# Optimization experiments

Measured on AMD Instinct MI355X. Metric: run time of the kernel, lower is better.

The kernel has to match this reference:

```python
import jax, jax.numpy as jnp
import numpy as np

K, M_EMB, N_HID, D_CTX, D_ATT, M_COV = 128, 256, 256, 684, 512, 256
B, H, W = 64, 16, 48


def gru_cell(x, h, W_ih, W_hh, b_ih, b_hh):
    # PyTorch GRUCell semantics
    gi = x @ W_ih.T + b_ih
    gh = h @ W_hh.T + b_hh
    i_r, i_z, i_n = jnp.split(gi, 3, axis=-1)
    h_r, h_z, h_n = jnp.split(gh, 3, axis=-1)
    r = jax.nn.sigmoid(i_r + h_r)
    z = jax.nn.sigmoid(i_z + h_z)
    n = jnp.tanh(i_n + r * h_n)
    return (1.0 - z) * n + z * h


def setup_inputs() -> dict:
    key = jax.random.key(0)
    ks = jax.random.split(key, 24)
    s = 0.02
    inp = {
        'y': jax.random.randint(ks[0], (B,), 0, K),
        'y_mask': jnp.ones((B,), jnp.float32),
        'context': jax.random.normal(ks[1], (B, D_CTX, H, W), jnp.float32),
        'pre_hidden': jax.random.normal(ks[2], (B, N_HID), jnp.float32),
        'alpha_past': jax.random.uniform(ks[3], (B, H, W), jnp.float32),
        'emb': jax.random.normal(ks[4], (K + 1, M_EMB)) * s,
        'W_ih1': jax.random.normal(ks[5], (3 * N_HID, M_EMB)) * s,
        'W_hh1': jax.random.normal(ks[6], (3 * N_HID, N_HID)) * s,
        'b_ih1': jnp.zeros((3 * N_HID,)),
        'b_hh1': jnp.zeros((3 * N_HID,)),
        'conv_Ua_w': jax.random.normal(ks[7], (D_ATT, D_CTX, 1, 1)) * s,
        'conv_Ua_b': jnp.zeros((D_ATT,)),
        'Wa': jax.random.normal(ks[8], (D_ATT, N_HID)) * s,
        'conv_Q_w': jax.random.normal(ks[9], (M_COV, 1, 3, 3)) * s,
        'Uf': jax.random.normal(ks[10], (D_ATT, M_COV)) * s,
        'Uf_b': jnp.zeros((D_ATT,)),
        'va': jax.random.normal(ks[11], (1, D_ATT)) * s,
        'va_b': jnp.zeros((1,)),
        'W_ih2': jax.random.normal(ks[12], (3 * N_HID, D_CTX)) * s,
        'W_hh2': jax.random.normal(ks[13], (3 * N_HID, N_HID)) * s,
        'b_ih2': jnp.zeros((3 * N_HID,)),
        'b_hh2': jnp.zeros((3 * N_HID,)),
        'Wct': jax.random.normal(ks[14], (M_EMB, D_CTX)) * s,
        'Wct_b': jnp.zeros((M_EMB,)),
        'Wht': jax.random.normal(ks[15], (M_EMB, N_HID)) * s,
        'Wht_b': jnp.zeros((M_EMB,)),
        'W0': jax.random.normal(ks[16], (K, M_EMB // 2)) * s,
        'W0_b': jnp.zeros((K,)),
    }
    return inp


def reference(y, y_mask, context, pre_hidden, alpha_past, emb,
              W_ih1, W_hh1, b_ih1, b_hh1, conv_Ua_w, conv_Ua_b, Wa,
              conv_Q_w, Uf, Uf_b, va, va_b,
              W_ih2, W_hh2, b_ih2, b_hh2, Wct, Wct_b, Wht, Wht_b, W0, W0_b):
    embedded = emb[y]                                           # [B, m]
    s_hat = gru_cell(embedded, pre_hidden, W_ih1, W_hh1, b_ih1, b_hh1)
    s_hat = y_mask[:, None] * s_hat + (1.0 - y_mask)[:, None] * pre_hidden

    Wa_h1 = s_hat @ Wa.T                                        # [B, A]
    # 1x1 conv == channel projection, output in NHWC layout
    Ua_ctx = jnp.einsum('bdhw,ad->bhwa', context, conv_Ua_w[:, :, 0, 0]) + conv_Ua_b
    # 3x3 coverage conv over past attention map
    cover_F = jax.lax.conv_general_dilated(
        alpha_past[:, None, :, :], conv_Q_w, (1, 1), 'SAME',
        dimension_numbers=('NCHW', 'OIHW', 'NCHW'))              # [B, M, H, W]
    cover_F = jnp.transpose(cover_F, (0, 2, 3, 1))               # [B, H, W, M]
    cover_vector = cover_F @ Uf.T + Uf_b                         # [B, H, W, A]

    e_att = jnp.tanh(Ua_ctx + Wa_h1[:, None, None, :] + cover_vector)
    alpha = (e_att @ va.T + va_b)[..., 0].reshape(e_att.shape[0], -1)  # [B, H*W]
    alpha = jax.nn.softmax(alpha, axis=1)

    ct = jnp.einsum('bdp,bp->bd', context.reshape(context.shape[0], context.shape[1], -1), alpha)

    s = gru_cell(ct, s_hat, W_ih2, W_hh2, b_ih2, b_hh2)
    s = y_mask[:, None] * s + (1.0 - y_mask)[:, None] * s_hat

    logit = ct @ Wct.T + Wct_b + s @ Wht.T + Wht_b + embedded    # [B, m]
    logit = logit.reshape(logit.shape[0], -1, 2).max(axis=2)     # maxout -> [B, m/2]
    out = logit @ W0.T + W0_b                                    # [B, K]
    return out, s, alpha.reshape(alpha.shape[0], H, W)
```

## Files before the change

### kernel.cpp

```cpp
#include <hip/hip_runtime.h>
#include <hip/hip_bf16.h>
#include <math.h>

#define BB 64
#define KV 128
#define ME 256
#define NH 256
#define DC 684
#define DA 512
#define MC 256
#define HH_ 16
#define WW_ 48
#define HW_ 768
#define NS 22

typedef __attribute__((ext_vector_type(8))) short bf16x8;
typedef __attribute__((ext_vector_type(4))) float f32x4;

#define WS_G     0
#define WS_RB    (WS_G + 4608)
#define WS_EMB   (WS_RB + 32768)
#define WS_SH    (WS_EMB + 16384)
#define WS_AL    (WS_SH + 16384)
#define WS_CT    (WS_AL + 49152)
#define WS_APACK (WS_CT + 43776)
#define WS_GI    (WS_APACK + 180224)
#define WS_GH    (WS_GI + 49152)
#define WS_LG    WS_GI
#define WS_BP    (WS_GH + 49152)
#define NEED_BYTES ((size_t)441600 * 4 + (size_t)34603008 * 2)

static __device__ __forceinline__ unsigned short f2b(float v) {
    __hip_bfloat16 h = __float2bfloat16(v);
    return *reinterpret_cast<unsigned short*>(&h);
}

static __device__ __forceinline__ void gl_lds16(const unsigned short* g,
                                                unsigned short* l) {
    __builtin_amdgcn_global_load_lds(
        (const __attribute__((address_space(1))) unsigned int*)g,
        (__attribute__((address_space(3))) unsigned int*)l, 16, 0, 0);
}

__global__ __launch_bounds__(512) void k_prep(
    const float* __restrict__ ctx, const float* __restrict__ Ua,
    const float* __restrict__ Uf, const float* __restrict__ convQ,
    const int* __restrict__ y, const float* __restrict__ emb,
    unsigned short* __restrict__ Bpack, unsigned short* __restrict__ Apack,
    float* __restrict__ G, float* __restrict__ embedded) {
    __shared__ unsigned short Ts[64 * 360];
    int bx = blockIdx.x, t = threadIdx.x;
    if (bx < 768) {
        int b = bx / 12, pt = bx % 12, p0 = pt * 64;
        int w = t >> 6, p = t & 63;
        unsigned short* dst = Bpack + (long)(b * 12 + pt) * 22 * 2048;
        for (int ch = 0; ch < 2; ch++) {
            int dbase = ch * 352;
            if (ch) __syncthreads();
#pragma unroll
            for (int iter = 0; iter < 11; iter++) {
                int d0 = dbase + iter * 32 + w * 4;
                float v0 = 0.f, v1 = 0.f, v2 = 0.f, v3 = 0.f;
                const float* src = ctx + ((long)b * DC + d0) * HW_ + p0 + p;
                if (d0 + 0 < DC) v0 = __builtin_nontemporal_load(src);
                if (d0 + 1 < DC) v1 = __builtin_nontemporal_load(src + HW_);
                if (d0 + 2 < DC) v2 = __builtin_nontemporal_load(src + 2 * HW_);
                if (d0 + 3 < DC) v3 = __builtin_nontemporal_load(src + 3 * HW_);
                unsigned u01 = (unsigned)f2b(v0) | ((unsigned)f2b(v1) << 16);
                unsigned u23 = (unsigned)f2b(v2) | ((unsigned)f2b(v3) << 16);
                *(uint2*)&Ts[p * 360 + (d0 - dbase)] = make_uint2(u01, u23);
            }
            __syncthreads();
            int so = t >> 8;
            int tt = t & 255;
            int pp = tt >> 2, slot = tt & 3;
#pragma unroll
            for (int s2 = 0; s2 < 12; s2 += 2) {
                int sl = s2 + so;
                if (sl < 11) {
                    int s = ch * 11 + sl;
                    bf16x8 v = *(const bf16x8*)&Ts[pp * 360 + sl * 32 +
                                                   ((slot ^ ((pp >> 1) & 3))
                                                    << 3)];
                    *(bf16x8*)(dst + (long)(s * 256 + tt) * 8) = v;
                }
            }
        }
    } else if (bx < 856) {
        int bi = bx - 768;
#pragma unroll
        for (int r = 0; r < 8; r++) {
            int idx = bi * 4096 + r * 512 + t;
            int e = idx & 7, slot = (idx >> 3) & 3;
            int a = (idx >> 5) & 511, s = idx >> 14;
            int d = s * 32 + ((slot ^ ((a >> 1) & 3)) << 3) + e;
            float v = (d < DC) ? Ua[a * DC + d] : 0.f;
            Apack[idx] = f2b(v);
        }
    } else if (bx < 865) {
        int idx = (bx - 856) * 512 + t;
        if (idx < DA * 9) {
            int a = idx / 9, k = idx % 9;
            float s = 0.f;
            for (int m = 0; m < MC; m++) s += Uf[a * MC + m] * convQ[m * 9 + k];
            G[idx] = s;
        }
    } else {
        int b = bx - 865;
        if (t < ME) embedded[b * ME + t] = emb[y[b] * ME + t];
    }
}

__global__ __launch_bounds__(256) void k_G(const float* __restrict__ Uf,
                                           const float* __restrict__ convQ,
                                           float* __restrict__ G) {
    int idx = blockIdx.x * 256 + threadIdx.x;
    if (idx >= DA * 9) return;
    int a = idx / 9, k = idx % 9;
    float s = 0.f;
    for (int m = 0; m < MC; m++) s += Uf[a * MC + m] * convQ[m * 9 + k];
    G[idx] = s;
}

__global__ __launch_bounds__(256) void k_prepA(const float* __restrict__ Ua,
                                               unsigned short* __restrict__ Apack) {
    int idx = blockIdx.x * 256 + threadIdx.x;
    if (idx >= NS * DA * 32) return;
    int e = idx & 7, slot = (idx >> 3) & 3;
    int a = (idx >> 5) & 511, s = idx >> 14;
    int d = s * 32 + ((slot ^ ((a >> 1) & 3)) << 3) + e;
    float v = (d < DC) ? Ua[a * DC + d] : 0.f;
    Apack[idx] = f2b(v);
}

__global__ __launch_bounds__(256) void k_emb(const int* __restrict__ y,
                                             const float* __restrict__ emb,
                                             float* __restrict__ embedded) {
    int b = blockIdx.x, t = threadIdx.x;
    embedded[b * ME + t] = emb[y[b] * ME + t];
}

__global__ __launch_bounds__(256) void k_rows256(
    const float* __restrict__ X, const float* __restrict__ W,
    const float* __restrict__ bias, const float* __restrict__ bias2,
    float* __restrict__ out, int outStride) {
    __shared__ float Xs[64 * 257];
    __shared__ float Ws[4 * 260];
    int t = threadIdx.x, w = t >> 6, lane = t & 63;
    for (int i = t; i < 64 * 256; i += 256) {
        int bb = i >> 8, k = i & 255;
        Xs[bb * 257 + k] = X[bb * 256 + k];
    }
    int r = blockIdx.x * 4 + w;
    *(f32x4*)(Ws + w * 260 + lane * 4) = *(const f32x4*)(W + r * 256 + lane * 4);
    __syncthreads();
    const float* xrow = Xs + lane * 257;
    const float* wrow = Ws + w * 260;
    float acc = 0.f;
#pragma unroll 8
    for (int k = 0; k < 256; k++) acc += wrow[k] * xrow[k];
    acc += bias[r];
    if (bias2) acc += bias2[r];
    out[lane * outStride + r] = acc;
}

__global__ __launch_bounds__(256) void k_gih1(
    const float* __restrict__ embedded, const float* __restrict__ pre_hidden,
    const float* __restrict__ W_ih1, const float* __restrict__ W_hh1,
    const float* __restrict__ b_ih1, const float* __restrict__ b_hh1,
    float* __restrict__ gi, float* __restrict__ gh) {
    __shared__ float Xs[64 * 257];
    __shared__ float Ws[4 * 260];
    int bx = blockIdx.x, t = threadIdx.x, w = t >> 6, lane = t & 63;
    const float *X, *W, *bias;
    float* outp;
    int r;
    if (bx < 192) {
        X = embedded; W = W_ih1; bias = b_ih1; outp = gi; r = bx * 4 + w;
    } else {
        X = pre_hidden; W = W_hh1; bias = b_hh1; outp = gh; r = (bx - 192) * 4 + w;
    }
    for (int i = t; i < 64 * 256; i += 256) {
        int bb = i >> 8, k = i & 255;
        Xs[bb * 257 + k] = X[bb * 256 + k];
    }
    *(f32x4*)(Ws + w * 260 + lane * 4) = *(const f32x4*)(W + r * 256 + lane * 4);
    __syncthreads();
    const float* xrow = Xs + lane * 257;
    const float* wrow = Ws + w * 260;
    float acc = 0.f;
#pragma unroll 8
    for (int k = 0; k < 256; k++) acc += wrow[k] * xrow[k];
    outp[lane * 768 + r] = acc + bias[r];
}

__global__ __launch_bounds__(256) void k_gih2(
    const float* __restrict__ ctv, const float* __restrict__ s_hat,
    const float* __restrict__ W_ih2, const float* __restrict__ W_hh2,
    const float* __restrict__ b_ih2, const float* __restrict__ b_hh2,
    float* __restrict__ gi, float* __restrict__ gh) {
    __shared__ float Xs[64 * 257];
    __shared__ float Ws[4 * 260];
    int bx = blockIdx.x, t = threadIdx.x, w = t >> 6, lane = t & 63;
    if (bx < 192) {
        int r = bx * 4 + w;
        float acc = 0.f;
        for (int c = 0; c < 3; c++) {
            int c0 = c * 228;
            __syncthreads();
            for (int i = t; i < 64 * 228; i += 256) {
                int bb = i / 228, kk = i - bb * 228;
                Xs[bb * 229 + kk] = ctv[bb * DC + c0 + kk];
            }
            for (int j = lane; j < 228; j += 64)
                Ws[w * 260 + j] = W_ih2[r * DC + c0 + j];
            __syncthreads();
            const float* xrow = Xs + lane * 229;
            const float* wrow = Ws + w * 260;
#pragma unroll 4
            for (int k = 0; k < 228; k++) acc += wrow[k] * xrow[k];
        }
        gi[lane * 768 + r] = acc + b_ih2[r];
    } else {
        int r = (bx - 192) * 4 + w;
        for (int i = t; i < 64 * 256; i += 256) {
            int bb = i >> 8, k = i & 255;
            Xs[bb * 257 + k] = s_hat[bb * 256 + k];
        }
        *(f32x4*)(Ws + w * 260 + lane * 4) =
            *(const f32x4*)(W_hh2 + r * 256 + lane * 4);
        __syncthreads();
        const float* xrow = Xs + lane * 257;
        const float* wrow = Ws + w * 260;
        float acc = 0.f;
#pragma unroll 8
        for (int k = 0; k < 256; k++) acc += wrow[k] * xrow[k];
        gh[lane * 768 + r] = acc + b_hh2[r];
    }
}

__global__ __launch_bounds__(256) void k_gru(const float* __restrict__ gi,
                                             const float* __restrict__ gh,
                                             const float* __restrict__ h,
                                             const float* __restrict__ y_mask,
                                             float* __restrict__ outp) {
    int b = blockIdx.x, t = threadIdx.x;
    float hv = h[b * NH + t];
    float r = 1.f / (1.f + expf(-(gi[b * 768 + t] + gh[b * 768 + t])));
    float z = 1.f / (1.f + expf(-(gi[b * 768 + 256 + t] + gh[b * 768 + 256 + t])));
    float n = tanhf(gi[b * 768 + 512 + t] + r * gh[b * 768 + 512 + t]);
    float sv = (1.f - z) * n + z * hv;
    float m = y_mask[b];
    outp[b * NH + t] = m * sv + (1.f - m) * hv;
}

__global__ __launch_bounds__(512) void k_att_gl(
    const unsigned short* __restrict__ Apack,
    const unsigned short* __restrict__ Bpack, const float* __restrict__ G,
    const float* __restrict__ rb, const float* __restrict__ va,
    const float* __restrict__ va_b, const float* __restrict__ apast,
    float* __restrict__ alogit) {
    __shared__ __attribute__((aligned(16))) unsigned short lsA[2][16384];
    __shared__ __attribute__((aligned(16))) unsigned short lsB[2][2048];
    __shared__ float ap_s[18 * 50];
    __shared__ float part_s[8][64];
    int pt = blockIdx.x, b = blockIdx.y;
    int t = threadIdx.x, w = t >> 6, lane = t & 63;
    int l15 = lane & 15, lg = lane >> 4;
    int sx = lg ^ ((l15 >> 1) & 3);

    for (int idx = t; idx < 900; idx += 512) {
        int hh = idx / 50, ww = idx % 50;
        float v = 0.f;
        if (hh >= 1 && hh <= HH_ && ww >= 1 && ww <= WW_)
            v = apast[b * HW_ + (hh - 1) * WW_ + (ww - 1)];
        ap_s[idx] = v;
    }

    const unsigned short* Asrc = Apack + w * 2048 + lane * 8;
    const unsigned short* Bsrc =
        Bpack + (long)(b * 12 + pt) * 22 * 2048 + w * 512 + lane * 8;

#define STAGE(S, BUF)                                                        \
    do {                                                                     \
        _Pragma("unroll") for (int i_ = 0; i_ < 4; i_++)                     \
            gl_lds16(Asrc + (long)(S)*16384 + i_ * 512,                      \
                     &lsA[BUF][w * 2048 + i_ * 512]);                        \
        if (w < 4) gl_lds16(Bsrc + (long)(S)*2048, &lsB[BUF][w * 512]);      \
    } while (0)

    f32x4 acc[4][4];
#pragma unroll
    for (int i = 0; i < 4; i++)
#pragma unroll
        for (int j = 0; j < 4; j++) acc[i][j] = {0.f, 0.f, 0.f, 0.f};

    STAGE(0, 0);
    __syncthreads();

    for (int s = 0; s < NS; s++) {
        int cur = s & 1;
        if (s + 1 < NS) STAGE(s + 1, cur ^ 1);
        bf16x8 af[4], bf[4];
#pragma unroll
        for (int j = 0; j < 4; j++)
            bf[j] = *(const bf16x8*)&lsB[cur][(j * 16 + l15) * 32 + sx * 8];
#pragma unroll
        for (int i = 0; i < 4; i++)
            af[i] = *(const bf16x8*)&lsA[cur][(w * 64 + i * 16 + l15) * 32 +
                                              sx * 8];
#pragma unroll
        for (int i = 0; i < 4; i++)
#pragma unroll
            for (int j = 0; j < 4; j++)
                acc[i][j] = __builtin_amdgcn_mfma_f32_16x16x32_bf16(
                    af[i], bf[j], acc[i][j], 0, 0, 0);
        __syncthreads();
    }
#undef STAGE

    float partial[4] = {0.f, 0.f, 0.f, 0.f};
#pragma unroll
    for (int i = 0; i < 4; i++) {
#pragma unroll
        for (int r = 0; r < 4; r++) {
            int a = w * 64 + i * 16 + lg * 4 + r;
            float rbv = rb[b * DA + a];
            float vav = va[a];
            const float* Ga = G + a * 9;
            float g0 = Ga[0], g1 = Ga[1], g2 = Ga[2], g3 = Ga[3], g4 = Ga[4];
            float g5 = Ga[5], g6 = Ga[6], g7 = Ga[7], g8 = Ga[8];
#pragma unroll
            for (int j = 0; j < 4; j++) {
                int p = pt * 64 + j * 16 + l15;
                int hh = p / WW_, ww = p % WW_;
                const float* ap = ap_s + hh * 50 + ww;
                float cov = g0 * ap[0] + g1 * ap[1] + g2 * ap[2] +
                            g3 * ap[50] + g4 * ap[51] + g5 * ap[52] +
                            g6 * ap[100] + g7 * ap[101] + g8 * ap[102];
                float e = tanhf(acc[i][j][r] + rbv + cov);
                partial[j] += vav * e;
            }
        }
    }
#pragma unroll
    for (int j = 0; j < 4; j++) {
        partial[j] += __shfl_xor(partial[j], 16);
        partial[j] += __shfl_xor(partial[j], 32);
    }
    if (lane < 16) {
#pragma unroll
        for (int j = 0; j < 4; j++) part_s[w][j * 16 + lane] = partial[j];
    }
    __syncthreads();
    if (t < 64) {
        float sum = va_b[0];
#pragma unroll
        for (int q = 0; q < 8; q++) sum += part_s[q][t];
        alogit[b * HW_ + pt * 64 + t] = sum;
    }
}

#define LDW 40
__global__ __launch_bounds__(256) void k_att_lds(
    const unsigned short* __restrict__ Apack, const float* __restrict__ ctx,
    const float* __restrict__ G, const float* __restrict__ rb,
    const float* __restrict__ va, const float* __restrict__ va_b,
    const float* __restrict__ apast, float* __restrict__ alogit) {
    __shared__ __attribute__((aligned(16))) short lsB[2][64 * LDW];
    __shared__ float ap_s[18 * 50];
    __shared__ float part_s[4 * 64];
    int b = blockIdx.y;
    int p0 = blockIdx.x * 64;
    int t = threadIdx.x;
    int w = t >> 6, lane = t & 63;
    int l15 = lane & 15, lg = lane >> 4;
    int sxA = lg ^ ((l15 >> 1) & 3);
    int pq = t & 15, kp = t >> 4;
    const float* ctx_b = ctx + (long)b * DC * HW_ + p0;

    for (int idx = t; idx < 900; idx += 256) {
        int hh = idx / 50, ww = idx % 50;
        float v = 0.f;
        if (hh >= 1 && hh <= HH_ && ww >= 1 && ww <= WW_)
            v = apast[b * HW_ + (hh - 1) * WW_ + (ww - 1)];
        ap_s[idx] = v;
    }

#define CTXLOAD(FA, FB, S)                                                   \
    do {                                                                     \
        int d_ = (S) * 32 + 2 * kp;                                          \
        const float* s0_ = ctx_b + (long)d_ * HW_ + pq;                      \
        bool g0_ = d_ < DC, g1_ = (d_ + 1) < DC;                             \
        _Pragma("unroll") for (int j_ = 0; j_ < 4; j_++) {                   \
            FA[j_] = g0_ ? s0_[16 * j_] : 0.f;                               \
            FB[j_] = g1_ ? s0_[HW_ + 16 * j_] : 0.f;                         \
        }                                                                    \
    } while (0)
#define STAGEW(FA, FB, BUF)                                                  \
    do {                                                                     \
        _Pragma("unroll") for (int j_ = 0; j_ < 4; j_++) {                   \
            ((unsigned*)lsB[BUF])[(pq + 16 * j_) * (LDW / 2) + kp] =         \
                (unsigned)f2b(FA[j_]) | ((unsigned)f2b(FB[j_]) << 16);       \
        }                                                                    \
    } while (0)
#define ALOAD(AF, S)                                                         \
    do {                                                                     \
        _Pragma("unroll") for (int i_ = 0; i_ < 8; i_++)                     \
            AF[i_] = *(const bf16x8*)(Apack +                                \
                ((long)((S)*512 + w * 128 + i_ * 16 + l15) * 4 + sxA) * 8);  \
    } while (0)
#define BREAD(BF, BUF)                                                       \
    do {                                                                     \
        _Pragma("unroll") for (int j_ = 0; j_ < 4; j_++)                     \
            BF[j_] = *(const bf16x8*)(&lsB[BUF][(j_ * 16 + l15) * LDW +      \
                                               lg * 8]);                     \
    } while (0)
#define MFMA8x4(AF, BF)                                                      \
    do {                                                                     \
        _Pragma("unroll") for (int i_ = 0; i_ < 8; i_++)                     \
            _Pragma("unroll") for (int j_ = 0; j_ < 4; j_++)                 \
                acc[i_][j_] = __builtin_amdgcn_mfma_f32_16x16x32_bf16(       \
                    AF[i_], BF[j_], acc[i_][j_], 0, 0, 0);                   \
    } while (0)

    f32x4 acc[8][4];
#pragma unroll
    for (int i = 0; i < 8; i++)
#pragma unroll
        for (int j = 0; j < 4; j++) acc[i][j] = {0.f, 0.f, 0.f, 0.f};

    float fa0[4], fb0[4], fa1[4], fb1[4];
    bf16x8 afr0[8], afr1[8], bfr[4];

    CTXLOAD(fa1, fb1, 0);
    ALOAD(afr0, 0);
    STAGEW(fa1, fb1, 0);
    CTXLOAD(fa1, fb1, 1);
    __syncthreads();

    for (int ss = 0; ss < NS; ss += 2) {
        if (ss + 2 < NS) CTXLOAD(fa0, fb0, ss + 2);
        ALOAD(afr1, ss + 1);
        BREAD(bfr, 0);
        STAGEW(fa1, fb1, 1);
        MFMA8x4(afr0, bfr);
        __syncthreads();
        if (ss + 3 < NS) CTXLOAD(fa1, fb1, ss + 3);
        if (ss + 2 < NS) {
            ALOAD(afr0, ss + 2);
            BREAD(bfr, 1);
            STAGEW(fa0, fb0, 0);
            MFMA8x4(afr1, bfr);
        } else {
            BREAD(bfr, 1);
            MFMA8x4(afr1, bfr);
        }
        __syncthreads();
    }

    float partial[4] = {0.f, 0.f, 0.f, 0.f};
#pragma unroll
    for (int i = 0; i < 8; i++) {
#pragma unroll
        for (int r = 0; r < 4; r++) {
            int a = w * 128 + i * 16 + lg * 4 + r;
            float rbv = rb[b * DA + a];
            float vav = va[a];
            const float* Ga = G + a * 9;
            float g0 = Ga[0], g1 = Ga[1], g2 = Ga[2], g3 = Ga[3], g4 = Ga[4];
            float g5 = Ga[5], g6 = Ga[6], g7 = Ga[7], g8 = Ga[8];
#pragma unroll
            for (int j = 0; j < 4; j++) {
                int p = p0 + j * 16 + l15;
                int hh = p / WW_, ww = p % WW_;
                const float* ap = ap_s + hh * 50 + ww;
                float cov = g0 * ap[0] + g1 * ap[1] + g2 * ap[2] +
                            g3 * ap[50] + g4 * ap[51] + g5 * ap[52] +
                            g6 * ap[100] + g7 * ap[101] + g8 * ap[102];
                float e = tanhf(acc[i][j][r] + rbv + cov);
                partial[j] += vav * e;
            }
        }
    }
#pragma unroll
    for (int j = 0; j < 4; j++) {
        partial[j] += __shfl_xor(partial[j], 16);
        partial[j] += __shfl_xor(partial[j], 32);
    }
    if (lane < 16) {
#pragma unroll
        for (int j = 0; j < 4; j++) part_s[w * 64 + j * 16 + lane] = partial[j];
    }
    __syncthreads();
    if (t < 64) {
        float s = va_b[0] + part_s[t] + part_s[64 + t] + part_s[128 + t] +
                  part_s[192 + t];
        alogit[b * HW_ + p0 + t] = s;
    }
}

__global__ __launch_bounds__(256) void k_softmax(const float* __restrict__ alogit,
                                                 float* __restrict__ alpha) {
    __shared__ float red[16];
    int b = blockIdx.x, t = threadIdx.x;
    float v[3];
    float mx = -1e30f;
    for (int i = 0; i < 3; i++) {
        v[i] = alogit[b * HW_ + i * 256 + t];
        mx = fmaxf(mx, v[i]);
    }
    for (int off = 32; off > 0; off >>= 1) mx = fmaxf(mx, __shfl_down(mx, off));
    if ((t & 63) == 0) red[t >> 6] = mx;
    __syncthreads();
    if (t == 0) red[0] = fmaxf(fmaxf(red[0], red[1]), fmaxf(red[2], red[3]));
    __syncthreads();
    mx = red[0];
    float sum = 0.f;
    for (int i = 0; i < 3; i++) {
        v[i] = expf(v[i] - mx);
        sum += v[i];
    }
    for (int off = 32; off > 0; off >>= 1) sum += __shfl_down(sum, off);
    if ((t & 63) == 0) red[8 + (t >> 6)] = sum;
    __syncthreads();
    if (t == 0) red[8] = red[8] + red[9] + red[10] + red[11];
    __syncthreads();
    float inv = 1.f / red[8];
    for (int i = 0; i < 3; i++) alpha[b * HW_ + i * 256 + t] = v[i] * inv;
}

__global__ __launch_bounds__(256) void k_ct_f32(const float* __restrict__ ctx,
                                                const float* __restrict__ alpha,
                                                float* __restrict__ ct) {
    __shared__ float al_s[HW_];
    int b = blockIdx.y;
    int dc0 = blockIdx.x * 114;
    int t = threadIdx.x;
    for (int i = t; i < HW_; i += 256) al_s[i] = alpha[b * HW_ + i];
    __syncthreads();
    int wave = t >> 6, lane = t & 63;
    for (int d = dc0 + wave; d < dc0 + 114; d += 4) {
        const float* row = &ctx[((long)b * DC + d) * HW_];
        float s = 0.f;
#pragma unroll
        for (int q = 0; q < 12; q++) s += row[lane + q * 64] * al_s[lane + q * 64];
        for (int off = 32; off > 0; off >>= 1) s += __shfl_down(s, off);
        if (lane == 0) ct[b * DC + d] = s;
    }
}

__global__ __launch_bounds__(256) void k_logit(
    const float* __restrict__ ctv, const float* __restrict__ s,
    const float* __restrict__ embedded, const float* __restrict__ Wct,
    const float* __restrict__ Wht, const float* __restrict__ Wct_b,
    const float* __restrict__ Wht_b, float* __restrict__ lg) {
    __shared__ float Xs[64 * 257];
    __shared__ float Ws[4 * 232];
    int t = threadIdx.x, w = t >> 6, lane = t & 63;
    int r = blockIdx.x * 4 + w;
    float acc = 0.f;
    for (int c = 0; c < 3; c++) {
        int c0 = c * 228;
        __syncthreads();
        for (int i = t; i < 64 * 228; i += 256) {
            int bb = i / 228, kk = i - bb * 228;
            Xs[bb * 229 + kk] = ctv[bb * DC + c0 + kk];
        }
        for (int j = lane; j < 228; j += 64) Ws[w * 232 + j] = Wct[r * DC + c0 + j];
        __syncthreads();
        const float* xrow = Xs + lane * 229;
        const float* wrow = Ws + w * 232;
#pragma unroll 4
        for (int k = 0; k < 228; k++) acc += wrow[k] * xrow[k];
    }
    __syncthreads();
    for (int i = t; i < 64 * 256; i += 256) {
        int bb = i >> 8, k = i & 255;
        Xs[bb * 257 + k] = s[bb * 256 + k];
    }
    __syncthreads();
    const float* xrow2 = Xs + lane * 257;
    const float* wr = Wht + r * 256;
    float acc2 = 0.f;
#pragma unroll 8
    for (int k = 0; k < 256; k++) acc2 += wr[k] * xrow2[k];
    lg[lane * 256 + r] = acc + acc2 + Wct_b[r] + Wht_b[r] + embedded[lane * 256 + r];
}

__global__ __launch_bounds__(256) void k_head(const float* __restrict__ lg,
                                              const float* __restrict__ W0,
                                              const float* __restrict__ W0_b,
                                              float* __restrict__ out) {
    __shared__ float Xs[64 * 129];
    __shared__ float Ws[4 * 132];
    int t = threadIdx.x, w = t >> 6, lane = t & 63;
    for (int i = t; i < 64 * 128; i += 256) {
        int bb = i >> 7, m = i & 127;
        Xs[bb * 129 + m] = fmaxf(lg[bb * 256 + 2 * m], lg[bb * 256 + 2 * m + 1]);
    }
    int r = blockIdx.x * 4 + w;
    Ws[w * 132 + lane] = W0[r * 128 + lane];
    Ws[w * 132 + 64 + lane] = W0[r * 128 + 64 + lane];
    __syncthreads();
    const float* xrow = Xs + lane * 129;
    const float* wrow = Ws + w * 132;
    float acc = 0.f;
#pragma unroll 8
    for (int k = 0; k < 128; k++) acc += wrow[k] * xrow[k];
    out[lane * KV + r] = acc + W0_b[r];
}

extern "C" void kernel_launch(void* const* d_in, const int* in_sizes, int n_in,
                              void* d_out, int out_size, void* d_ws,
                              size_t ws_size, hipStream_t stream) {
    const int* y = (const int*)d_in[0];
    const float* y_mask = (const float*)d_in[1];
    const float* context = (const float*)d_in[2];
    const float* pre_hidden = (const float*)d_in[3];
    const float* alpha_past = (const float*)d_in[4];
    const float* emb = (const float*)d_in[5];
    const float* W_ih1 = (const float*)d_in[6];
    const float* W_hh1 = (const float*)d_in[7];
    const float* b_ih1 = (const float*)d_in[8];
    const float* b_hh1 = (const float*)d_in[9];
    const float* conv_Ua_w = (const float*)d_in[10];
    const float* conv_Ua_b = (const float*)d_in[11];
    const float* Wa = (const float*)d_in[12];
    const float* conv_Q_w = (const float*)d_in[13];
    const float* Uf = (const float*)d_in[14];
    const float* Uf_b = (const float*)d_in[15];
    const float* va = (const float*)d_in[16];
    const float* va_b = (const float*)d_in[17];
    const float* W_ih2 = (const float*)d_in[18];
    const float* W_hh2 = (const float*)d_in[19];
    const float* b_ih2 = (const float*)d_in[20];
    const float* b_hh2 = (const float*)d_in[21];
    const float* Wct = (const float*)d_in[22];
    const float* Wct_b = (const float*)d_in[23];
    const float* Wht = (const float*)d_in[24];
    const float* Wht_b = (const float*)d_in[25];
    const float* W0 = (const float*)d_in[26];
    const float* W0_b = (const float*)d_in[27];

    float* ws = (float*)d_ws;
    float* out = (float*)d_out;
    float* G = ws + WS_G;
    float* rbias = ws + WS_RB;
    float* embedded = ws + WS_EMB;
    float* s_hat = ws + WS_SH;
    float* alogit = ws + WS_AL;
    float* ctv = ws + WS_CT;
    unsigned short* Apack = (unsigned short*)(ws + WS_APACK);
    float* gi = ws + WS_GI;
    float* gh = ws + WS_GH;
    float* lg = ws + WS_LG;
    unsigned short* Bpack = (unsigned short*)(ws + WS_BP);
    float* s_out = out + 8192;
    float* alpha_out = out + 24576;

    bool fast = ws_size >= NEED_BYTES;

    if (fast) {
        k_prep<<<dim3(929), dim3(512), 0, stream>>>(context, conv_Ua_w, Uf,
                                                    conv_Q_w, y, emb, Bpack,
                                                    Apack, G, embedded);
    } else {
        k_G<<<dim3(18), dim3(256), 0, stream>>>(Uf, conv_Q_w, G);
        k_prepA<<<dim3((NS * DA * 32 + 255) / 256), dim3(256), 0, stream>>>(
            conv_Ua_w, Apack);
        k_emb<<<dim3(64), dim3(256), 0, stream>>>(y, emb, embedded);
    }
    k_gih1<<<dim3(384), dim3(256), 0, stream>>>(embedded, pre_hidden, W_ih1,
                                                W_hh1, b_ih1, b_hh1, gi, gh);
    k_gru<<<dim3(64), dim3(256), 0, stream>>>(gi, gh, pre_hidden, y_mask, s_hat);
    k_rows256<<<dim3(128), dim3(256), 0, stream>>>(s_hat, Wa, conv_Ua_b, Uf_b,
                                                   rbias, 512);
    if (fast) {
        k_att_gl<<<dim3(12, 64), dim3(512), 0, stream>>>(
            Apack, Bpack, G, rbias, va, va_b, alpha_past, alogit);
    } else {
        k_att_lds<<<dim3(12, 64), dim3(256), 0, stream>>>(
            Apack, context, G, rbias, va, va_b, alpha_past, alogit);
    }
    k_softmax<<<dim3(64), dim3(256), 0, stream>>>(alogit, alpha_out);
    k_ct_f32<<<dim3(6, 64), dim3(256), 0, stream>>>(context, alpha_out, ctv);
    k_gih2<<<dim3(384), dim3(256), 0, stream>>>(ctv, s_hat, W_ih2, W_hh2, b_ih2,
                                                b_hh2, gi, gh);
    k_gru<<<dim3(64), dim3(256), 0, stream>>>(gi, gh, s_hat, y_mask, s_out);
    k_logit<<<dim3(64), dim3(256), 0, stream>>>(ctv, s_out, embedded, Wct, Wht,
                                                Wct_b, Wht_b, lg);
    k_head<<<dim3(32), dim3(256), 0, stream>>>(lg, W0, W0_b, out);
}
```

Before: 257.7 us.

## Deepen attention GEMM prefetch with vmcnt waits and fuse softmax into context reduction

The attention GEMM kernel now keeps two stages in flight. It waits with explicit s_waitcnt vmcnt counts and raw barriers instead of a full __syncthreads per step, and all 8 waves issue B loads so every wave has the same counter. Softmax is fused into the ct reduction kernel: each of the 6 blocks per batch recomputes the softmax and only block 0 writes alpha, which removes one launch and an alpha round trip. The context reads in prep drop the nontemporal hint. The main risk is that the hand-set vmcnt values are fragile if the compiler reorders loads, and the softmax work is now repeated six times.

```diff
diff --git a/kernel.cpp b/kernel.cpp
--- a/kernel.cpp
+++ b/kernel.cpp
@@ -62,10 +62,10 @@
                 int d0 = dbase + iter * 32 + w * 4;
                 float v0 = 0.f, v1 = 0.f, v2 = 0.f, v3 = 0.f;
                 const float* src = ctx + ((long)b * DC + d0) * HW_ + p0 + p;
-                if (d0 + 0 < DC) v0 = __builtin_nontemporal_load(src);
-                if (d0 + 1 < DC) v1 = __builtin_nontemporal_load(src + HW_);
-                if (d0 + 2 < DC) v2 = __builtin_nontemporal_load(src + 2 * HW_);
-                if (d0 + 3 < DC) v3 = __builtin_nontemporal_load(src + 3 * HW_);
+                if (d0 + 0 < DC) v0 = src[0];
+                if (d0 + 1 < DC) v1 = src[HW_];
+                if (d0 + 2 < DC) v2 = src[2 * HW_];
+                if (d0 + 3 < DC) v3 = src[3 * HW_];
                 unsigned u01 = (unsigned)f2b(v0) | ((unsigned)f2b(v1) << 16);
                 unsigned u23 = (unsigned)f2b(v2) | ((unsigned)f2b(v3) << 16);
                 *(uint2*)&Ts[p * 360 + (d0 - dbase)] = make_uint2(u01, u23);
@@ -254,7 +254,7 @@
     outp[b * NH + t] = m * sv + (1.f - m) * hv;
 }
 
-__global__ __launch_bounds__(512) void k_att_gl(
+__global__ __launch_bounds__(512) void k_att_cnt(
     const unsigned short* __restrict__ Apack,
     const unsigned short* __restrict__ Bpack, const float* __restrict__ G,
     const float* __restrict__ rb, const float* __restrict__ va,
@@ -276,19 +276,34 @@
             v = apast[b * HW_ + (hh - 1) * WW_ + (ww - 1)];
         ap_s[idx] = v;
     }
+    __syncthreads();
 
     const unsigned short* Asrc = Apack + w * 2048 + lane * 8;
     const unsigned short* Bsrc =
-        Bpack + (long)(b * 12 + pt) * 22 * 2048 + w * 512 + lane * 8;
+        Bpack + (long)(b * 12 + pt) * 22 * 2048 + (w & 3) * 512 + lane * 8;
 
 #define STAGE(S, BUF)                                                        \
     do {                                                                     \
         _Pragma("unroll") for (int i_ = 0; i_ < 4; i_++)                     \
             gl_lds16(Asrc + (long)(S)*16384 + i_ * 512,                      \
                      &lsA[BUF][w * 2048 + i_ * 512]);                        \
-        if (w < 4) gl_lds16(Bsrc + (long)(S)*2048, &lsB[BUF][w * 512]);      \
+        gl_lds16(Bsrc + (long)(S)*2048, &lsB[BUF][(w & 3) * 512]);           \
     } while (0)
 
+#define STEP_BODY(CUR)                                                       \
+    do {                                                                     \
+        bf16x8 af[4], bf[4];                                                 \
+        _Pragma("unroll") for (int j = 0; j < 4; j++)                        \
+            bf[j] = *(const bf16x8*)&lsB[CUR][(j * 16 + l15) * 32 + sx * 8]; \
+        _Pragma("unroll") for (int i = 0; i < 4; i++)                        \
+            af[i] = *(const bf16x8*)&lsA[CUR][(w * 64 + i * 16 + l15) * 32 + \
+                                             sx * 8];                        \
+        _Pragma("unroll") for (int i = 0; i < 4; i++)                        \
+            _Pragma("unroll") for (int j = 0; j < 4; j++)                    \
+                acc[i][j] = __builtin_amdgcn_mfma_f32_16x16x32_bf16(         \
+                    af[i], bf[j], acc[i][j], 0, 0, 0);                       \
+    } while (0)
+
     f32x4 acc[4][4];
 #pragma unroll
     for (int i = 0; i < 4; i++)
@@ -296,28 +311,26 @@
         for (int j = 0; j < 4; j++) acc[i][j] = {0.f, 0.f, 0.f, 0.f};
 
     STAGE(0, 0);
-    __syncthreads();
-
-    for (int s = 0; s < NS; s++) {
+    STAGE(1, 1);
+
+    for (int s = 0; s < NS - 1; s++) {
         int cur = s & 1;
-        if (s + 1 < NS) STAGE(s + 1, cur ^ 1);
-        bf16x8 af[4], bf[4];
-#pragma unroll
-        for (int j = 0; j < 4; j++)
-            bf[j] = *(const bf16x8*)&lsB[cur][(j * 16 + l15) * 32 + sx * 8];
-#pragma unroll
-        for (int i = 0; i < 4; i++)
-            af[i] = *(const bf16x8*)&lsA[cur][(w * 64 + i * 16 + l15) * 32 +
-                                              sx * 8];
-#pragma unroll
-        for (int i = 0; i < 4; i++)
-#pragma unroll
-            for (int j = 0; j < 4; j++)
-                acc[i][j] = __builtin_amdgcn_mfma_f32_16x16x32_bf16(
-                    af[i], bf[j], acc[i][j], 0, 0, 0);
-        __syncthreads();
-    }
+        asm volatile("s_waitcnt vmcnt(5)" ::: "memory");
+        __builtin_amdgcn_sched_barrier(0);
+        __builtin_amdgcn_s_barrier();
+        __builtin_amdgcn_sched_barrier(0);
+        STEP_BODY(cur);
+        __builtin_amdgcn_s_barrier();
+        __builtin_amdgcn_sched_barrier(0);
+        if (s + 2 < NS) STAGE(s + 2, cur);
+    }
+    asm volatile("s_waitcnt vmcnt(0)" ::: "memory");
+    __builtin_amdgcn_sched_barrier(0);
+    __builtin_amdgcn_s_barrier();
+    __builtin_amdgcn_sched_barrier(0);
+    STEP_BODY((NS - 1) & 1);
 #undef STAGE
+#undef STEP_BODY
 
     float partial[4] = {0.f, 0.f, 0.f, 0.f};
 #pragma unroll
@@ -500,10 +513,13 @@
     }
 }
 
-__global__ __launch_bounds__(256) void k_softmax(const float* __restrict__ alogit,
-                                                 float* __restrict__ alpha) {
+__global__ __launch_bounds__(256) void k_ctsm(const float* __restrict__ ctx,
+                                              const float* __restrict__ alogit,
+                                              float* __restrict__ ct,
+                                              float* __restrict__ alpha_out) {
+    __shared__ float al_s[HW_];
     __shared__ float red[16];
-    int b = blockIdx.x, t = threadIdx.x;
+    int b = blockIdx.y, t = threadIdx.x;
     float v[3];
     float mx = -1e30f;
     for (int i = 0; i < 3; i++) {
@@ -527,18 +543,13 @@
     if (t == 0) red[8] = red[8] + red[9] + red[10] + red[11];
     __syncthreads();
     float inv = 1.f / red[8];
-    for (int i = 0; i < 3; i++) alpha[b * HW_ + i * 256 + t] = v[i] * inv;
-}
-
-__global__ __launch_bounds__(256) void k_ct_f32(const float* __restrict__ ctx,
-                                                const float* __restrict__ alpha,
-                                                float* __restrict__ ct) {
-    __shared__ float al_s[HW_];
-    int b = blockIdx.y;
+    for (int i = 0; i < 3; i++) {
+        float a = v[i] * inv;
+        al_s[i * 256 + t] = a;
+        if (blockIdx.x == 0) alpha_out[b * HW_ + i * 256 + t] = a;
+    }
+    __syncthreads();
     int dc0 = blockIdx.x * 114;
-    int t = threadIdx.x;
-    for (int i = t; i < HW_; i += 256) al_s[i] = alpha[b * HW_ + i];
-    __syncthreads();
     int wave = t >> 6, lane = t & 63;
     for (int d = dc0 + wave; d < dc0 + 114; d += 4) {
         const float* row = &ctx[((long)b * DC + d) * HW_];
@@ -677,14 +688,14 @@
     k_rows256<<<dim3(128), dim3(256), 0, stream>>>(s_hat, Wa, conv_Ua_b, Uf_b,
                                                    rbias, 512);
     if (fast) {
-        k_att_gl<<<dim3(12, 64), dim3(512), 0, stream>>>(
+        k_att_cnt<<<dim3(12, 64), dim3(512), 0, stream>>>(
             Apack, Bpack, G, rbias, va, va_b, alpha_past, alogit);
     } else {
         k_att_lds<<<dim3(12, 64), dim3(256), 0, stream>>>(
             Apack, context, G, rbias, va, va_b, alpha_past, alogit);
     }
-    k_softmax<<<dim3(64), dim3(256), 0, stream>>>(alogit, alpha_out);
-    k_ct_f32<<<dim3(6, 64), dim3(256), 0, stream>>>(context, alpha_out, ctv);
+    k_ctsm<<<dim3(6, 64), dim3(256), 0, stream>>>(context, alogit, ctv,
+                                                  alpha_out);
     k_gih2<<<dim3(384), dim3(256), 0, stream>>>(ctv, s_hat, W_ih2, W_hh2, b_ih2,
                                                 b_hh2, gi, gh);
     k_gru<<<dim3(64), dim3(256), 0, stream>>>(gi, gh, s_hat, y_mask, s_out);
```

Measured after the change: 247.7 us. -3.9%, faster.
